# Kernel optimization log

Measured on AMD Instinct MI355X. Metric: run time of the kernel, lower is better.

Reference implementation:

```python
import jax, jax.numpy as jnp
import numpy as np
from jax import lax

B, N, D, OUT = 256, 4096, 512, 512
EPS = 1e-5
NPOINT = 128  # 4 modalities * 32 tokens each


def setup_inputs() -> dict:
    key = jax.random.key(0)
    ks = jax.random.split(key, 32)
    f32 = jnp.float32
    nrm = lambda k, s, sc=0.05: jax.random.normal(k, s, f32) * sc
    inp = {
        'rgb': jax.random.normal(ks[0], (B, 49, D), f32),
        'depth': jax.random.normal(ks[1], (B, 49, D), f32),
        'mmwave': jax.random.normal(ks[2], (B, 32, D), f32),
        'lidar': jax.random.normal(ks[3], (B, 32, D), f32),
        'lidar_points': jax.random.normal(ks[4], (B, N, 3), f32),
        # per-modality conv1d(k=1) weights, stacked [rgb, depth, mmwave, lidar]
        'conv_w': nrm(ks[5], (4, OUT, D)),
        'conv_b': nrm(ks[6], (4, OUT)),
        # eval-mode BatchNorm1d params per modality
        'bn_g': 1.0 + nrm(ks[7], (4, OUT)),
        'bn_b': nrm(ks[8], (4, OUT)),
        'bn_m': nrm(ks[9], (4, OUT)),
        'bn_v': 0.5 + jax.random.uniform(ks[10], (4, OUT), f32),
        # nn.Linear(49,32) for rgb/depth, nn.Linear(32,32) for mmwave/lidar
        'lin_w_img': nrm(ks[11], (2, 32, 49)),
        'lin_b_img': nrm(ks[12], (2, 32)),
        'lin_w_pc': nrm(ks[13], (2, 32, 32)),
        'lin_b_pc': nrm(ks[14], (2, 32)),
        # pos_enc_layer: Conv1d(3,128,1)+BN+ReLU, Conv1d(128,OUT,1)+BN+ReLU
        'pe_w1': nrm(ks[15], (128, 3)),
        'pe_b1': nrm(ks[16], (128,)),
        'pe_g1': 1.0 + nrm(ks[17], (128,)),
        'pe_bb1': nrm(ks[18], (128,)),
        'pe_m1': nrm(ks[19], (128,)),
        'pe_v1': 0.5 + jax.random.uniform(ks[20], (128,), f32),
        'pe_w2': nrm(ks[21], (OUT, 128)),
        'pe_b2': nrm(ks[22], (OUT,)),
        'pe_g2': 1.0 + nrm(ks[23], (OUT,)),
        'pe_bb2': nrm(ks[24], (OUT,)),
        'pe_m2': nrm(ks[25], (OUT,)),
        'pe_v2': 0.5 + jax.random.uniform(ks[26], (OUT,), f32),
    }
    return inp


def _bn(x, g, b, m, v):
    # x: [B, C, L]; eval-mode batchnorm over channel dim
    return (x - m[:, None]) * (g / jnp.sqrt(v + EPS))[:, None] + b[:, None]


def _branch(x, cw, cb, g, bb, m, v, lw, lb):
    # x: [B, L, D] (already the un-permuted feature); conv1d(k=1) == matmul
    h = jnp.einsum('bld,od->bol', x, cw) + cb[:, None]  # [B, OUT, L]
    h = jax.nn.relu(_bn(h, g, bb, m, v))
    h = jnp.einsum('bol,kl->bok', h, lw) + lb           # Linear on last dim -> [B, OUT, 32]
    return jax.nn.relu(h)


def _fps(xyz, npoint):
    # faithful farthest point sampling: npoint sequential iterations as lax.scan
    Bb, Nn, _ = xyz.shape
    far0 = jax.random.randint(jax.random.key(42), (Bb,), 0, Nn)
    dist0 = jnp.full((Bb, Nn), 1e10, xyz.dtype)
    def step(carry, _):
        distance, farthest = carry
        idx = jnp.broadcast_to(farthest[:, None, None], (Bb, 1, 3))
        centroid = jnp.take_along_axis(xyz, idx, axis=1)      # [B,1,3]
        d = jnp.sum((xyz - centroid) ** 2, -1)                # [B,N]
        distance = jnp.minimum(distance, d)
        return (distance, jnp.argmax(distance, -1)), farthest
    _, idxs = lax.scan(step, (dist0, far0), None, length=npoint)
    return jnp.transpose(idxs)  # [B, npoint]


def reference(rgb, depth, mmwave, lidar, lidar_points,
              conv_w, conv_b, bn_g, bn_b, bn_m, bn_v,
              lin_w_img, lin_b_img, lin_w_pc, lin_b_pc,
              pe_w1, pe_b1, pe_g1, pe_bb1, pe_m1, pe_v1,
              pe_w2, pe_b2, pe_g2, pe_bb2, pe_m2, pe_v2):
    # active_modalities = ['rgb','depth','mmwave','lidar']
    feats = [
        _branch(rgb,    conv_w[0], conv_b[0], bn_g[0], bn_b[0], bn_m[0], bn_v[0], lin_w_img[0], lin_b_img[0]),
        _branch(depth,  conv_w[1], conv_b[1], bn_g[1], bn_b[1], bn_m[1], bn_v[1], lin_w_img[1], lin_b_img[1]),
        _branch(mmwave, conv_w[2], conv_b[2], bn_g[2], bn_b[2], bn_m[2], bn_v[2], lin_w_pc[0], lin_b_pc[0]),
        _branch(lidar,  conv_w[3], conv_b[3], bn_g[3], bn_b[3], bn_m[3], bn_v[3], lin_w_pc[1], lin_b_pc[1]),
    ]
    proj = jnp.transpose(jnp.concatenate(feats, axis=2), (0, 2, 1))  # [B, 128, OUT]
    S = proj.shape[1]
    fps_idx = _fps(lidar_points, S)                                   # [B, S]
    gi = jnp.broadcast_to(fps_idx[..., None], (lidar_points.shape[0], S, 3))
    new_xyz = jnp.take_along_axis(lidar_points, gi, axis=1)           # [B, S, 3]
    h = jnp.einsum('bsd,od->bos', new_xyz, pe_w1) + pe_b1[:, None]    # [B,128,S]
    h = jax.nn.relu(_bn(h, pe_g1, pe_bb1, pe_m1, pe_v1))
    h = jnp.einsum('bcs,oc->bos', h, pe_w2) + pe_b2[:, None]          # [B,OUT,S]
    h = jax.nn.relu(_bn(h, pe_g2, pe_bb2, pe_m2, pe_v2))
    return proj + jnp.transpose(h, (0, 2, 1))
```

## Files before the change

### kernel.cpp

```cpp
#include <hip/hip_runtime.h>
#include <stdint.h>

typedef unsigned int u32;
typedef unsigned short u16;

typedef __attribute__((ext_vector_type(8))) short bf16x8;
typedef __attribute__((ext_vector_type(8))) unsigned short u16x8;
typedef __attribute__((ext_vector_type(4))) float f32x4;

__device__ __forceinline__ u16 f2bfu(float f) {
  union { float f; u32 u; } v; v.f = f;
  return (u16)((v.u + 0x7FFFu + ((v.u >> 16) & 1u)) >> 16);
}

__device__ __forceinline__ void gload16(const void* g, void* l) {
  __builtin_amdgcn_global_load_lds(
      (const __attribute__((address_space(1))) void*)g,
      (__attribute__((address_space(3))) void*)l, 16, 0, 0);
}

__device__ __forceinline__ u32 rotl32(u32 x, int r) { return (x << r) | (x >> (32 - r)); }

__device__ __forceinline__ uint2 threefry2x32(u32 k0, u32 k1, u32 x0, u32 x1) {
  u32 ks2 = k0 ^ k1 ^ 0x1BD11BDAu;
  x0 += k0; x1 += k1;
#define TF_G(a,b,c,d) { x0 += x1; x1 = rotl32(x1,a); x1 ^= x0; \
                        x0 += x1; x1 = rotl32(x1,b); x1 ^= x0; \
                        x0 += x1; x1 = rotl32(x1,c); x1 ^= x0; \
                        x0 += x1; x1 = rotl32(x1,d); x1 ^= x0; }
  TF_G(13,15,26,6);  x0 += k1;  x1 += ks2 + 1u;
  TF_G(17,29,16,24); x0 += ks2; x1 += k0  + 2u;
  TF_G(13,15,26,6);  x0 += k0;  x1 += k1  + 3u;
  TF_G(17,29,16,24); x0 += k1;  x1 += ks2 + 4u;
  TF_G(13,15,26,6);  x0 += ks2; x1 += k0  + 5u;
#undef TF_G
  return make_uint2(x0, x1);
}

__global__ __launch_bounds__(256) void convert_kernel(
    const float* __restrict__ rgb, const float* __restrict__ depth,
    const float* __restrict__ mmw, const float* __restrict__ lid,
    const float* __restrict__ conv_w, u16* __restrict__ Wc, u16* __restrict__ Xc)
{
  const int bid = blockIdx.x, tid = threadIdx.x;
  float4 v0 = make_float4(0.f, 0.f, 0.f, 0.f), v1 = v0;
  char* dst;
  if (bid < 12288) {
    const int y = bid >> 4, ks = bid & 15;
    const int l = tid >> 2, seg = tid & 3;
    const float* xp; size_t row = 0; bool valid = true;
    if (y < 256)      { xp = rgb;   row = (size_t)y * 49 + l;         valid = (l < 49); }
    else if (y < 512) { xp = depth; row = (size_t)(y - 256) * 49 + l; valid = (l < 49); }
    else if (y < 640) { xp = mmw;   row = (size_t)(y - 512) * 64 + l; }
    else              { xp = lid;   row = (size_t)(y - 640) * 64 + l; }
    if (valid) {
      const float* s = xp + row * 512 + ks * 32 + seg * 8;
      v0 = *(const float4*)s; v1 = *(const float4*)(s + 4);
    }
    dst = (char*)Xc + (size_t)y * 65536 + ks * 4096 + l * 64 + ((seg ^ ((l >> 1) & 3)) << 4);
  } else {
    const int t = bid - 12288;
    const int tile = t >> 1, half = t & 1;
    const int row = (tid >> 2) + half * 64, seg = tid & 3;
    const float* s = conv_w + (size_t)((tile >> 4) * 128 + row) * 512 + (tile & 15) * 32 + seg * 8;
    v0 = *(const float4*)s; v1 = *(const float4*)(s + 4);
    dst = (char*)Wc + (size_t)tile * 8192 + row * 64 + ((seg ^ ((row >> 1) & 3)) << 4);
  }
  u16x8 pk;
  pk[0] = f2bfu(v0.x); pk[1] = f2bfu(v0.y); pk[2] = f2bfu(v0.z); pk[3] = f2bfu(v0.w);
  pk[4] = f2bfu(v1.x); pk[5] = f2bfu(v1.y); pk[6] = f2bfu(v1.z); pk[7] = f2bfu(v1.w);
  *(u16x8*)dst = pk;
}

#define FSMEM_SZ 52864

__global__ __launch_bounds__(256) void fused_kernel(
    const float* __restrict__ pts, int* __restrict__ fps_idx,
    const u16* __restrict__ Wc, const u16* __restrict__ Xc,
    const float* __restrict__ conv_b,
    const float* __restrict__ bn_g, const float* __restrict__ bn_b,
    const float* __restrict__ bn_m, const float* __restrict__ bn_v,
    const float* __restrict__ lin_w_img, const float* __restrict__ lin_b_img,
    const float* __restrict__ lin_w_pc, const float* __restrict__ lin_b_pc,
    float* __restrict__ out)
{
  __shared__ __align__(16) char sm[FSMEM_SZ];
  const int tid = threadIdx.x;

  if (blockIdx.x < 256) {
    float* xs = (float*)sm;
    float* ys = (float*)(sm + 16384);
    float* zs = (float*)(sm + 32768);
    float* rv2 = (float*)(sm + 49152);
    int*   ri2 = (int*)(sm + 49184);
    const int b = blockIdx.x;
    const float* pb = pts + (size_t)b * 4096 * 3;

    __builtin_amdgcn_s_setprio(1);

    for (int i = tid; i < 12288; i += 256) {
      float v = pb[i];
      int n = i / 3, c = i - n * 3;
      float* dstp = (c == 0) ? xs : (c == 1) ? ys : zs;
      dstp[n] = v;
    }
    __syncthreads();

    float xr[16], yr[16], zr[16], dreg[16];
#pragma unroll
    for (int i = 0; i < 16; i++) {
      int n = tid + (i << 8);
      xr[i] = xs[n]; yr[i] = ys[n]; zr[i] = zs[n];
      dreg[i] = 1e10f;
    }

    uint2 k2 = threefry2x32(0u, 42u, 0u, 1u);
    uint2 r  = threefry2x32(k2.x, k2.y, 0u, (u32)b);
    int far  = (int)((r.x ^ r.y) & 4095u);
    const int wv = tid >> 6;

    for (int s = 0; s < 128; s++) {
      if (tid == 0) fps_idx[b * 128 + s] = far;
      float cx = xs[far], cy = ys[far], cz = zs[far];
      float bv[16]; int bn[16];
#pragma unroll
      for (int i = 0; i < 16; i++) {
        float dx = __fsub_rn(xr[i], cx);
        float dy = __fsub_rn(yr[i], cy);
        float dz = __fsub_rn(zr[i], cz);
        float d  = __fadd_rn(__fadd_rn(__fmul_rn(dx, dx), __fmul_rn(dy, dy)), __fmul_rn(dz, dz));
        float nd = fminf(dreg[i], d);
        dreg[i] = nd;
        bv[i] = nd; bn[i] = tid + (i << 8);
      }
#define MRG(i, j) if (bv[j] > bv[i]) { bv[i] = bv[j]; bn[i] = bn[j]; }
      MRG(0, 8)  MRG(1, 9)  MRG(2, 10) MRG(3, 11)
      MRG(4, 12) MRG(5, 13) MRG(6, 14) MRG(7, 15)
      MRG(0, 4)  MRG(1, 5)  MRG(2, 6)  MRG(3, 7)
      MRG(0, 2)  MRG(1, 3)
      MRG(0, 1)
#undef MRG
      float bestv = bv[0]; int besti = bn[0];
#pragma unroll
      for (int off = 1; off < 64; off <<= 1) {
        float ov = __shfl_xor(bestv, off, 64);
        int   oi = __shfl_xor(besti, off, 64);
        if (ov > bestv || (ov == bestv && oi < besti)) { bestv = ov; besti = oi; }
      }
      const int par = s & 1;
      if ((tid & 63) == 0) { rv2[par * 4 + wv] = bestv; ri2[par * 4 + wv] = besti; }
      __syncthreads();
      float bvv = rv2[par * 4]; int bii = ri2[par * 4];
#pragma unroll
      for (int w2 = 1; w2 < 4; w2++) {
        float wvv = rv2[par * 4 + w2]; int wii = ri2[par * 4 + w2];
        if (wvv > bvv || (wvv == bvv && wii < bii)) { bvv = wvv; bii = wii; }
      }
      far = bii;
    }
    return;
  }

  const int g  = (int)blockIdx.x - 256;
  const int ot = g & 3;
  const int y  = g >> 2;
  int mod, bidx = 0, bg = 0;
  if      (y < 256) { mod = 0; bidx = y; }
  else if (y < 512) { mod = 1; bidx = y - 256; }
  else if (y < 640) { mod = 2; bg   = y - 512; }
  else              { mod = 3; bg   = y - 640; }
  const bool img = (mod < 2);
  const int  L   = img ? 49 : 32;
  const float* lw = img ? (lin_w_img + mod * 32 * 49) : (lin_w_pc + (mod - 2) * 32 * 32);
  const float* lb = img ? (lin_b_img + mod * 32)      : (lin_b_pc + (mod - 2) * 32);

  u16*   lw2 = (u16*)(sm + 47104);
  float* bnA = (float*)(sm + 51712);
  float* bnC = (float*)(sm + 52224);
  float* lbs = (float*)(sm + 52736);
  u16*   hsB = (u16*)(sm + 24576);
  float* Cb  = (float*)sm;

  for (int i = tid; i < 32 * 64; i += 256) {
    int kk = i >> 6, l = i & 63;
    float v = (l < L) ? lw[kk * L + l] : 0.f;
    lw2[kk * 72 + l] = f2bfu(v);
  }
  if (tid < 32) lbs[tid] = lb[tid];
  if (tid < 128) {
    int o = mod * 512 + ot * 128 + tid;
    float sc = bn_g[o] / sqrtf(bn_v[o] + 1e-5f);
    bnA[tid] = sc;
    bnC[tid] = (conv_b[o] - bn_m[o]) * sc + bn_b[o];
  }

  const int lane = tid & 63, w = tid >> 6, quad = lane >> 4, lm = lane & 15;
  const int xorq = ((lm >> 1) & 3) << 4;
  const int soff = w * 1024 + lane * 16;

  const char* wcB = (const char*)Wc + (size_t)(mod * 4 + ot) * (16 * 8192);
  const char* xcB = (const char*)Xc + (size_t)y * 65536;

  f32x4 acc[2][4];
#pragma unroll
  for (int mi = 0; mi < 2; mi++)
#pragma unroll
    for (int nt = 0; nt < 4; nt++) acc[mi][nt] = (f32x4){0.f, 0.f, 0.f, 0.f};

  asm volatile("s_waitcnt vmcnt(0)" ::: "memory");
  gload16(wcB + soff,        sm + soff);
  gload16(wcB + soff + 4096, sm + soff + 4096);
  gload16(xcB + soff,        sm + 16384 + soff);

#pragma unroll
  for (int ks = 0; ks < 16; ks++) {
    const int cur = ks & 1;
    if (ks < 15) {
      const char* wsrc = wcB + (ks + 1) * 8192;
      const char* xsrc = xcB + (ks + 1) * 4096;
      char* wd = sm + (cur ^ 1) * 8192;
      char* xd = sm + 16384 + (cur ^ 1) * 4096;
      gload16(wsrc + soff,        wd + soff);
      gload16(wsrc + soff + 4096, wd + soff + 4096);
      gload16(xsrc + soff,        xd + soff);
      asm volatile("s_waitcnt vmcnt(3)" ::: "memory");
    } else {
      asm volatile("s_waitcnt vmcnt(0)" ::: "memory");
    }
    __builtin_amdgcn_s_barrier();
    asm volatile("" ::: "memory");
    const char* wbc = sm + cur * 8192;
    const char* xbc = sm + 16384 + cur * 4096;
    bf16x8 af[2], bfr[4];
#pragma unroll
    for (int mi = 0; mi < 2; mi++)
      af[mi] = *(const bf16x8*)(wbc + w * 2048 + mi * 1024 + lm * 64 + ((quad * 16) ^ xorq));
#pragma unroll
    for (int nt = 0; nt < 4; nt++)
      bfr[nt] = *(const bf16x8*)(xbc + nt * 1024 + lm * 64 + ((quad * 16) ^ xorq));
#pragma unroll
    for (int mi = 0; mi < 2; mi++)
#pragma unroll
      for (int nt = 0; nt < 4; nt++)
        acc[mi][nt] = __builtin_amdgcn_mfma_f32_16x16x32_bf16(af[mi], bfr[nt], acc[mi][nt], 0, 0, 0);
    asm volatile("s_waitcnt lgkmcnt(0)" ::: "memory");
    __builtin_amdgcn_s_barrier();
  }

#pragma unroll
  for (int mi = 0; mi < 2; mi++)
#pragma unroll
    for (int nt = 0; nt < 4; nt++)
#pragma unroll
      for (int r = 0; r < 4; r++) {
        int o_loc = w * 32 + mi * 16 + quad * 4 + r;
        int l     = nt * 16 + lm;
        float v = acc[mi][nt][r] * bnA[o_loc] + bnC[o_loc];
        hsB[o_loc * 88 + l] = f2bfu(v > 0.f ? v : 0.f);
      }
  __syncthreads();

  const int npass = img ? 1 : 2;
  const int nkt   = img ? 2 : 1;
  for (int p = 0; p < npass; p++) {
    f32x4 c2[2][2];
#pragma unroll
    for (int mi = 0; mi < 2; mi++)
#pragma unroll
      for (int nt2 = 0; nt2 < 2; nt2++) c2[mi][nt2] = (f32x4){0.f, 0.f, 0.f, 0.f};
    for (int kt = 0; kt < nkt; kt++) {
      int aoff = img ? kt * 32 : p * 32;
      int boff = img ? kt * 32 : 0;
      bf16x8 a2[2], b2[2];
#pragma unroll
      for (int mi = 0; mi < 2; mi++)
        a2[mi] = *(const bf16x8*)&hsB[(w * 32 + mi * 16 + lm) * 88 + aoff + quad * 8];
#pragma unroll
      for (int nt2 = 0; nt2 < 2; nt2++)
        b2[nt2] = *(const bf16x8*)&lw2[(nt2 * 16 + lm) * 72 + boff + quad * 8];
#pragma unroll
      for (int mi = 0; mi < 2; mi++)
#pragma unroll
        for (int nt2 = 0; nt2 < 2; nt2++)
          c2[mi][nt2] = __builtin_amdgcn_mfma_f32_16x16x32_bf16(a2[mi], b2[nt2], c2[mi][nt2], 0, 0, 0);
    }
#pragma unroll
    for (int mi = 0; mi < 2; mi++)
#pragma unroll
      for (int nt2 = 0; nt2 < 2; nt2++)
#pragma unroll
        for (int r = 0; r < 4; r++) {
          int kk    = nt2 * 16 + lm;
          int o_loc = w * 32 + mi * 16 + quad * 4 + r;
          float v = c2[mi][nt2][r] + lbs[kk];
          Cb[kk * 132 + o_loc] = v > 0.f ? v : 0.f;
        }
    __syncthreads();
    int b_out = img ? bidx : (bg * 2 + p);
    for (int i = tid; i < 4096; i += 256) {
      int kk = i >> 7, j = i & 127;
      out[((size_t)b_out * 128 + mod * 32 + kk) * 512 + ot * 128 + j] = Cb[kk * 132 + j];
    }
    if (p + 1 < npass) __syncthreads();
  }
}

#define WB_OFF   0
#define XB_OFF   8192
#define CB_OFF   0
#define HS_OFF   16896
#define LW2_OFF  39424
#define BNA_OFF  44032
#define BNC_OFF  44544
#define LBS_OFF  45056
#define SMEM_SZ  45184

__global__ __launch_bounds__(256) void branch_kernel(
    const float* __restrict__ x0p, const float* __restrict__ x1p,
    const float* __restrict__ x2p, const float* __restrict__ x3p,
    const float* __restrict__ conv_w, const float* __restrict__ conv_b,
    const float* __restrict__ bn_g, const float* __restrict__ bn_b,
    const float* __restrict__ bn_m, const float* __restrict__ bn_v,
    const float* __restrict__ lin_w_img, const float* __restrict__ lin_b_img,
    const float* __restrict__ lin_w_pc, const float* __restrict__ lin_b_pc,
    float* __restrict__ out)
{
  __shared__ __align__(16) char sm[SMEM_SZ];
  u16*   Wb  = (u16*)(sm + WB_OFF);
  u16*   Xb  = (u16*)(sm + XB_OFF);
  float* Cb  = (float*)(sm + CB_OFF);
  u16*   hsB = (u16*)(sm + HS_OFF);
  u16*   lw2 = (u16*)(sm + LW2_OFF);
  float* bnA = (float*)(sm + BNA_OFF);
  float* bnC = (float*)(sm + BNC_OFF);
  float* lbs = (float*)(sm + LBS_OFF);

  const int ot  = blockIdx.x;
  const int tid = threadIdx.x;
  int y = blockIdx.y;
  int mod, bidx = 0, bg = 0;
  if      (y < 256) { mod = 0; bidx = y; }
  else if (y < 512) { mod = 1; bidx = y - 256; }
  else if (y < 640) { mod = 2; bg   = y - 512; }
  else              { mod = 3; bg   = y - 640; }
  const bool img = (mod < 2);
  const int  L   = img ? 49 : 32;
  const float* xp = (mod == 0) ? x0p : (mod == 1) ? x1p : (mod == 2) ? x2p : x3p;
  const float* lw = img ? (lin_w_img + mod * 32 * 49) : (lin_w_pc + (mod - 2) * 32 * 32);
  const float* lb = img ? (lin_b_img + mod * 32)      : (lin_b_pc + (mod - 2) * 32);

  for (int i = tid; i < 32 * 64; i += 256) {
    int kk = i >> 6, l = i & 63;
    float v = (l < L) ? lw[kk * L + l] : 0.f;
    lw2[kk * 72 + l] = f2bfu(v);
  }
  if (tid < 32) lbs[tid] = lb[tid];
  if (tid < 128) {
    int o = mod * 512 + ot * 128 + tid;
    float sc = bn_g[o] / sqrtf(bn_v[o] + 1e-5f);
    bnA[tid] = sc;
    bnC[tid] = (conv_b[o] - bn_m[o]) * sc + bn_b[o];
  }

  const int lane = tid & 63, w = tid >> 6, quad = lane >> 4, lm = lane & 15;
  const float* wbase = conv_w + (size_t)(mod * 512 + ot * 128) * 512;

  f32x4 acc[2][4];
#pragma unroll
  for (int mi = 0; mi < 2; mi++)
#pragma unroll
    for (int nt = 0; nt < 4; nt++) acc[mi][nt] = (f32x4){0.f, 0.f, 0.f, 0.f};

  for (int ks = 0; ks < 16; ks++) {
    int k0 = ks * 32;
    __syncthreads();
    for (int i = tid; i < 1024; i += 256) {
      int row = i >> 3, seg = i & 7;
      float4 v = *(const float4*)(wbase + (size_t)row * 512 + k0 + seg * 4);
      u16* d = &Wb[row * 32 + seg * 4];
      d[0] = f2bfu(v.x); d[1] = f2bfu(v.y); d[2] = f2bfu(v.z); d[3] = f2bfu(v.w);
    }
    for (int i = tid; i < 512; i += 256) {
      int l = i >> 3, seg = i & 7;
      float4 v = make_float4(0.f, 0.f, 0.f, 0.f);
      if (img) {
        if (l < 49) v = *(const float4*)(xp + (size_t)(bidx * 49 + l) * 512 + k0 + seg * 4);
      } else {
        v = *(const float4*)(xp + (size_t)(bg * 64 + l) * 512 + k0 + seg * 4);
      }
      u16* d = &Xb[l * 32 + seg * 4];
      d[0] = f2bfu(v.x); d[1] = f2bfu(v.y); d[2] = f2bfu(v.z); d[3] = f2bfu(v.w);
    }
    __syncthreads();
    bf16x8 af[2], bfr[4];
#pragma unroll
    for (int mi = 0; mi < 2; mi++)
      af[mi] = *(const bf16x8*)&Wb[(w * 32 + mi * 16 + lm) * 32 + quad * 8];
#pragma unroll
    for (int nt = 0; nt < 4; nt++)
      bfr[nt] = *(const bf16x8*)&Xb[(nt * 16 + lm) * 32 + quad * 8];
#pragma unroll
    for (int mi = 0; mi < 2; mi++)
#pragma unroll
      for (int nt = 0; nt < 4; nt++)
        acc[mi][nt] = __builtin_amdgcn_mfma_f32_16x16x32_bf16(af[mi], bfr[nt], acc[mi][nt], 0, 0, 0);
  }
  __syncthreads();

#pragma unroll
  for (int mi = 0; mi < 2; mi++)
#pragma unroll
    for (int nt = 0; nt < 4; nt++)
#pragma unroll
      for (int r = 0; r < 4; r++) {
        int o_loc = w * 32 + mi * 16 + quad * 4 + r;
        int l     = nt * 16 + lm;
        float v = acc[mi][nt][r] * bnA[o_loc] + bnC[o_loc];
        hsB[o_loc * 88 + l] = f2bfu(v > 0.f ? v : 0.f);
      }
  __syncthreads();

  const int npass = img ? 1 : 2;
  const int nkt   = img ? 2 : 1;
  for (int p = 0; p < npass; p++) {
    f32x4 c2[2][2];
#pragma unroll
    for (int mi = 0; mi < 2; mi++)
#pragma unroll
      for (int nt2 = 0; nt2 < 2; nt2++) c2[mi][nt2] = (f32x4){0.f, 0.f, 0.f, 0.f};
    for (int kt = 0; kt < nkt; kt++) {
      int aoff = img ? kt * 32 : p * 32;
      int boff = img ? kt * 32 : 0;
      bf16x8 a2[2], b2[2];
#pragma unroll
      for (int mi = 0; mi < 2; mi++)
        a2[mi] = *(const bf16x8*)&hsB[(w * 32 + mi * 16 + lm) * 88 + aoff + quad * 8];
#pragma unroll
      for (int nt2 = 0; nt2 < 2; nt2++)
        b2[nt2] = *(const bf16x8*)&lw2[(nt2 * 16 + lm) * 72 + boff + quad * 8];
#pragma unroll
      for (int mi = 0; mi < 2; mi++)
#pragma unroll
        for (int nt2 = 0; nt2 < 2; nt2++)
          c2[mi][nt2] = __builtin_amdgcn_mfma_f32_16x16x32_bf16(a2[mi], b2[nt2], c2[mi][nt2], 0, 0, 0);
    }
#pragma unroll
    for (int mi = 0; mi < 2; mi++)
#pragma unroll
      for (int nt2 = 0; nt2 < 2; nt2++)
#pragma unroll
        for (int r = 0; r < 4; r++) {
          int kk    = nt2 * 16 + lm;
          int o_loc = w * 32 + mi * 16 + quad * 4 + r;
          float v = c2[mi][nt2][r] + lbs[kk];
          Cb[kk * 132 + o_loc] = v > 0.f ? v : 0.f;
        }
    __syncthreads();
    int b_out = img ? bidx : (bg * 2 + p);
    for (int i = tid; i < 4096; i += 256) {
      int kk = i >> 7, j = i & 127;
      out[((size_t)b_out * 128 + mod * 32 + kk) * 512 + ot * 128 + j] = Cb[kk * 132 + j];
    }
    if (p + 1 < npass) __syncthreads();
  }
}

__global__ __launch_bounds__(256) void fps_kernel(const float* __restrict__ pts,
                                                  int* __restrict__ idx_out)
{
  __shared__ float xs[4096], ys[4096], zs[4096];
  __shared__ float rv[4];
  __shared__ int   ri[4];
  __shared__ int   far_sh;
  const int b = blockIdx.x, tid = threadIdx.x;
  const float* pb = pts + (size_t)b * 4096 * 3;

  for (int i = tid; i < 12288; i += 256) {
    float v = pb[i];
    int n = i / 3, c = i - n * 3;
    float* dst = (c == 0) ? xs : (c == 1) ? ys : zs;
    dst[n] = v;
  }
  float dreg[16];
#pragma unroll
  for (int i = 0; i < 16; i++) dreg[i] = 1e10f;
  __syncthreads();

  uint2 k2 = threefry2x32(0u, 42u, 0u, 1u);
  uint2 r  = threefry2x32(k2.x, k2.y, 0u, (u32)b);
  int far  = (int)((r.x ^ r.y) & 4095u);

  for (int s = 0; s < 128; s++) {
    if (tid == 0) idx_out[b * 128 + s] = far;
    float cx = xs[far], cy = ys[far], cz = zs[far];
    float bestv = -1.f; int besti = 0x7FFFFFFF;
#pragma unroll
    for (int i = 0; i < 16; i++) {
      int n = tid + (i << 8);
      float dx = __fsub_rn(xs[n], cx);
      float dy = __fsub_rn(ys[n], cy);
      float dz = __fsub_rn(zs[n], cz);
      float d  = __fadd_rn(__fadd_rn(__fmul_rn(dx, dx), __fmul_rn(dy, dy)), __fmul_rn(dz, dz));
      float nd = fminf(dreg[i], d);
      dreg[i] = nd;
      if (nd > bestv) { bestv = nd; besti = n; }
    }
#pragma unroll
    for (int off = 1; off < 64; off <<= 1) {
      float ov = __shfl_xor(bestv, off, 64);
      int   oi = __shfl_xor(besti, off, 64);
      if (ov > bestv || (ov == bestv && oi < besti)) { bestv = ov; besti = oi; }
    }
    if ((tid & 63) == 0) { rv[tid >> 6] = bestv; ri[tid >> 6] = besti; }
    __syncthreads();
    if (tid == 0) {
      float bv = rv[0]; int bi = ri[0];
#pragma unroll
      for (int w = 1; w < 4; w++)
        if (rv[w] > bv || (rv[w] == bv && ri[w] < bi)) { bv = rv[w]; bi = ri[w]; }
      far_sh = bi;
    }
    __syncthreads();
    far = far_sh;
  }
}

__global__ __launch_bounds__(256) void pe_kernel(
    const float* __restrict__ pts, const int* __restrict__ fps_idx,
    const float* __restrict__ w1, const float* __restrict__ b1,
    const float* __restrict__ g1, const float* __restrict__ bb1,
    const float* __restrict__ m1, const float* __restrict__ v1,
    const float* __restrict__ w2, const float* __restrict__ b2,
    const float* __restrict__ g2, const float* __restrict__ bb2,
    const float* __restrict__ m2, const float* __restrict__ v2,
    float* __restrict__ out)
{
  __shared__ float h1T[64][132];
  __shared__ float w2s[64][132];
  __shared__ float sc1s[128], C1s[128];
  const int ot = blockIdx.x;
  const int st = blockIdx.y;
  const int b  = blockIdx.z;
  const int tid = threadIdx.x;

  for (int i = tid; i < 64 * 32; i += 256) {
    int o = i >> 5, j = i & 31;
    float4 v = *(const float4*)(w2 + (size_t)(ot * 64 + o) * 128 + j * 4);
    *(float4*)&w2s[o][j * 4] = v;
  }
  if (tid < 128) {
    float sc = g1[tid] / sqrtf(v1[tid] + 1e-5f);
    sc1s[tid] = sc;
    C1s[tid]  = (b1[tid] - m1[tid]) * sc + bb1[tid];
  }
  __syncthreads();

  {
    int s_l = tid & 63;
    int cq  = tid >> 6;
    int s   = st * 64 + s_l;
    int n   = fps_idx[b * 128 + s];
    float px = pts[((size_t)b * 4096 + n) * 3 + 0];
    float py = pts[((size_t)b * 4096 + n) * 3 + 1];
    float pz = pts[((size_t)b * 4096 + n) * 3 + 2];
    for (int cc = 0; cc < 32; cc++) {
      int c = cq * 32 + cc;
      float d  = fmaf(pz, w1[c * 3 + 2], fmaf(py, w1[c * 3 + 1], px * w1[c * 3]));
      float h  = d * sc1s[c] + C1s[c];
      h1T[s_l][c] = h > 0.f ? h : 0.f;
    }
  }
  __syncthreads();

  const int tx = tid & 15, ty = tid >> 4;
  float acc[4][4];
#pragma unroll
  for (int j = 0; j < 4; j++)
#pragma unroll
    for (int i = 0; i < 4; i++) acc[j][i] = 0.f;

  for (int c = 0; c < 128; c += 4) {
    float4 wv[4];
#pragma unroll
    for (int j = 0; j < 4; j++) wv[j] = *(const float4*)&w2s[tx + 16 * j][c];
#pragma unroll
    for (int si = 0; si < 4; si++) {
      float4 hv = *(const float4*)&h1T[ty + 16 * si][c];
#pragma unroll
      for (int j = 0; j < 4; j++) {
        acc[j][si] = fmaf(hv.x, wv[j].x, acc[j][si]);
        acc[j][si] = fmaf(hv.y, wv[j].y, acc[j][si]);
        acc[j][si] = fmaf(hv.z, wv[j].z, acc[j][si]);
        acc[j][si] = fmaf(hv.w, wv[j].w, acc[j][si]);
      }
    }
  }

#pragma unroll
  for (int j = 0; j < 4; j++) {
    int o = ot * 64 + tx + 16 * j;
    float sc = g2[o] / sqrtf(v2[o] + 1e-5f);
    float C  = (b2[o] - m2[o]) * sc + bb2[o];
#pragma unroll
    for (int si = 0; si < 4; si++) {
      int s = st * 64 + ty + 16 * si;
      float v = acc[j][si] * sc + C;
      v = v > 0.f ? v : 0.f;
      size_t oi = ((size_t)b * 128 + s) * 512 + o;
      out[oi] = out[oi] + v;
    }
  }
}

extern "C" void kernel_launch(void* const* d_in, const int* in_sizes, int n_in,
                              void* d_out, int out_size, void* d_ws, size_t ws_size,
                              hipStream_t stream) {
  const float* rgb    = (const float*)d_in[0];
  const float* depth  = (const float*)d_in[1];
  const float* mmwave = (const float*)d_in[2];
  const float* lidar  = (const float*)d_in[3];
  const float* pts    = (const float*)d_in[4];
  const float* conv_w = (const float*)d_in[5];
  const float* conv_b = (const float*)d_in[6];
  const float* bn_g   = (const float*)d_in[7];
  const float* bn_b   = (const float*)d_in[8];
  const float* bn_m   = (const float*)d_in[9];
  const float* bn_v   = (const float*)d_in[10];
  const float* lwi    = (const float*)d_in[11];
  const float* lbi    = (const float*)d_in[12];
  const float* lwp    = (const float*)d_in[13];
  const float* lbp    = (const float*)d_in[14];
  const float* pw1    = (const float*)d_in[15];
  const float* pb1    = (const float*)d_in[16];
  const float* pg1    = (const float*)d_in[17];
  const float* pbb1   = (const float*)d_in[18];
  const float* pm1    = (const float*)d_in[19];
  const float* pv1    = (const float*)d_in[20];
  const float* pw2    = (const float*)d_in[21];
  const float* pb2    = (const float*)d_in[22];
  const float* pg2    = (const float*)d_in[23];
  const float* pbb2   = (const float*)d_in[24];
  const float* pm2    = (const float*)d_in[25];
  const float* pv2    = (const float*)d_in[26];
  float* out = (float*)d_out;
  int* fps_idx = (int*)d_ws;

  const size_t NEED = 131072 + 2097152 + (size_t)768 * 65536;
  if (ws_size >= NEED) {
    u16* Wc = (u16*)((char*)d_ws + 131072);
    u16* Xc = (u16*)((char*)d_ws + 2228224);
    convert_kernel<<<dim3(12800), 256, 0, stream>>>(rgb, depth, mmwave, lidar,
        conv_w, Wc, Xc);
    fused_kernel<<<dim3(3328), 256, 0, stream>>>(pts, fps_idx, Wc, Xc,
        conv_b, bn_g, bn_b, bn_m, bn_v, lwi, lbi, lwp, lbp, out);
  } else {
    branch_kernel<<<dim3(4, 768), 256, 0, stream>>>(rgb, depth, mmwave, lidar,
        conv_w, conv_b, bn_g, bn_b, bn_m, bn_v, lwi, lbi, lwp, lbp, out);
    fps_kernel<<<dim3(256), 256, 0, stream>>>(pts, fps_idx);
  }
  pe_kernel<<<dim3(8, 2, 256), 256, 0, stream>>>(pts, fps_idx, pw1, pb1, pg1, pbb1, pm1, pv1,
      pw2, pb2, pg2, pbb2, pm2, pv2, out);
}
```

Before: 444.7 us.

## Move positional-encoding MLP to split-bf16 MFMA and use DPP for FPS argmax

Replaces the scalar positional-encoding kernel with an MFMA kernel. It splits the hidden activations and the second-layer weights into hi/lo bf16 pairs and does three bf16 MFMAs per tile to stay close to fp32 accuracy. The convert kernel now also precomputes the hi/lo weights and the folded BN scale/shift vectors. The FPS wave-level argmax reduction swaps shuffle-xor for DPP row ops plus a readlane, to cut latency on the serial FPS critical path. This adds workspace use and a 3x MFMA count.

```diff
diff --git a/kernel.cpp b/kernel.cpp
--- a/kernel.cpp
+++ b/kernel.cpp
@@ -11,12 +11,25 @@
 __device__ __forceinline__ u16 f2bfu(float f) {
   union { float f; u32 u; } v; v.f = f;
   return (u16)((v.u + 0x7FFFu + ((v.u >> 16) & 1u)) >> 16);
+}
+__device__ __forceinline__ float bf2f(u16 h) {
+  union { u32 u; float f; } v; v.u = ((u32)h) << 16;
+  return v.f;
 }
 
 __device__ __forceinline__ void gload16(const void* g, void* l) {
   __builtin_amdgcn_global_load_lds(
       (const __attribute__((address_space(1))) void*)g,
       (__attribute__((address_space(3))) void*)l, 16, 0, 0);
+}
+
+template <int CTRL>
+__device__ __forceinline__ void dpp_merge(float& bv, int& bi) {
+  int ovi = __builtin_amdgcn_update_dpp(__float_as_int(bv), __float_as_int(bv),
+                                        CTRL, 0xF, 0xF, false);
+  int oii = __builtin_amdgcn_update_dpp(bi, bi, CTRL, 0xF, 0xF, false);
+  float ov = __int_as_float(ovi);
+  if (ov > bv || (ov == bv && oii < bi)) { bv = ov; bi = oii; }
 }
 
 __device__ __forceinline__ u32 rotl32(u32 x, int r) { return (x << r) | (x >> (32 - r)); }
@@ -40,12 +53,20 @@
 __global__ __launch_bounds__(256) void convert_kernel(
     const float* __restrict__ rgb, const float* __restrict__ depth,
     const float* __restrict__ mmw, const float* __restrict__ lid,
-    const float* __restrict__ conv_w, u16* __restrict__ Wc, u16* __restrict__ Xc)
+    const float* __restrict__ conv_w, u16* __restrict__ Wc, u16* __restrict__ Xc,
+    const float* __restrict__ pw2,
+    const float* __restrict__ pg1, const float* __restrict__ pbb1,
+    const float* __restrict__ pm1, const float* __restrict__ pv1,
+    const float* __restrict__ pb1,
+    const float* __restrict__ pg2, const float* __restrict__ pbb2,
+    const float* __restrict__ pm2, const float* __restrict__ pv2,
+    const float* __restrict__ pb2,
+    u16* __restrict__ W2h, u16* __restrict__ W2l,
+    float* __restrict__ sc1C1, float* __restrict__ sc2C2)
 {
   const int bid = blockIdx.x, tid = threadIdx.x;
-  float4 v0 = make_float4(0.f, 0.f, 0.f, 0.f), v1 = v0;
-  char* dst;
   if (bid < 12288) {
+    float4 v0 = make_float4(0.f, 0.f, 0.f, 0.f), v1 = v0;
     const int y = bid >> 4, ks = bid & 15;
     const int l = tid >> 2, seg = tid & 3;
     const float* xp; size_t row = 0; bool valid = true;
@@ -57,19 +78,48 @@
       const float* s = xp + row * 512 + ks * 32 + seg * 8;
       v0 = *(const float4*)s; v1 = *(const float4*)(s + 4);
     }
-    dst = (char*)Xc + (size_t)y * 65536 + ks * 4096 + l * 64 + ((seg ^ ((l >> 1) & 3)) << 4);
-  } else {
+    char* dst = (char*)Xc + (size_t)y * 65536 + ks * 4096 + l * 64 + ((seg ^ ((l >> 1) & 3)) << 4);
+    u16x8 pk;
+    pk[0] = f2bfu(v0.x); pk[1] = f2bfu(v0.y); pk[2] = f2bfu(v0.z); pk[3] = f2bfu(v0.w);
+    pk[4] = f2bfu(v1.x); pk[5] = f2bfu(v1.y); pk[6] = f2bfu(v1.z); pk[7] = f2bfu(v1.w);
+    *(u16x8*)dst = pk;
+  } else if (bid < 12800) {
     const int t = bid - 12288;
     const int tile = t >> 1, half = t & 1;
     const int row = (tid >> 2) + half * 64, seg = tid & 3;
     const float* s = conv_w + (size_t)((tile >> 4) * 128 + row) * 512 + (tile & 15) * 32 + seg * 8;
-    v0 = *(const float4*)s; v1 = *(const float4*)(s + 4);
-    dst = (char*)Wc + (size_t)tile * 8192 + row * 64 + ((seg ^ ((row >> 1) & 3)) << 4);
-  }
-  u16x8 pk;
-  pk[0] = f2bfu(v0.x); pk[1] = f2bfu(v0.y); pk[2] = f2bfu(v0.z); pk[3] = f2bfu(v0.w);
-  pk[4] = f2bfu(v1.x); pk[5] = f2bfu(v1.y); pk[6] = f2bfu(v1.z); pk[7] = f2bfu(v1.w);
-  *(u16x8*)dst = pk;
+    float4 v0 = *(const float4*)s; float4 v1 = *(const float4*)(s + 4);
+    char* dst = (char*)Wc + (size_t)tile * 8192 + row * 64 + ((seg ^ ((row >> 1) & 3)) << 4);
+    u16x8 pk;
+    pk[0] = f2bfu(v0.x); pk[1] = f2bfu(v0.y); pk[2] = f2bfu(v0.z); pk[3] = f2bfu(v0.w);
+    pk[4] = f2bfu(v1.x); pk[5] = f2bfu(v1.y); pk[6] = f2bfu(v1.z); pk[7] = f2bfu(v1.w);
+    *(u16x8*)dst = pk;
+  } else if (bid < 12832) {
+    const int idx = (bid - 12800) * 2048 + tid * 8;
+    const float* s = pw2 + idx;
+    float4 v0 = *(const float4*)s; float4 v1 = *(const float4*)(s + 4);
+    float vv[8] = {v0.x, v0.y, v0.z, v0.w, v1.x, v1.y, v1.z, v1.w};
+    u16x8 hh, hl;
+#pragma unroll
+    for (int j = 0; j < 8; j++) {
+      u16 hi = f2bfu(vv[j]);
+      hh[j] = hi;
+      hl[j] = f2bfu(vv[j] - bf2f(hi));
+    }
+    *(u16x8*)(W2h + idx) = hh;
+    *(u16x8*)(W2l + idx) = hl;
+  } else {
+    if (tid < 128) {
+      float sc = pg1[tid] / sqrtf(pv1[tid] + 1e-5f);
+      sc1C1[tid]       = sc;
+      sc1C1[128 + tid] = (pb1[tid] - pm1[tid]) * sc + pbb1[tid];
+    }
+    for (int o = tid; o < 512; o += 256) {
+      float sc = pg2[o] / sqrtf(pv2[o] + 1e-5f);
+      sc2C2[o]       = sc;
+      sc2C2[512 + o] = (pb2[o] - pm2[o]) * sc + pbb2[o];
+    }
+  }
 }
 
 #define FSMEM_SZ 52864
@@ -141,14 +191,17 @@
       MRG(0, 1)
 #undef MRG
       float bestv = bv[0]; int besti = bn[0];
-#pragma unroll
-      for (int off = 1; off < 64; off <<= 1) {
-        float ov = __shfl_xor(bestv, off, 64);
-        int   oi = __shfl_xor(besti, off, 64);
-        if (ov > bestv || (ov == bestv && oi < besti)) { bestv = ov; besti = oi; }
-      }
+      dpp_merge<0x111>(bestv, besti);
+      dpp_merge<0x112>(bestv, besti);
+      dpp_merge<0x114>(bestv, besti);
+      dpp_merge<0x118>(bestv, besti);
+      dpp_merge<0x142>(bestv, besti);
+      dpp_merge<0x143>(bestv, besti);
+      float wbv = __int_as_float(__builtin_amdgcn_readlane(__float_as_int(bestv), 63));
+      int   wbi = __builtin_amdgcn_readlane(besti, 63);
+
       const int par = s & 1;
-      if ((tid & 63) == 0) { rv2[par * 4 + wv] = bestv; ri2[par * 4 + wv] = besti; }
+      if ((tid & 63) == 0) { rv2[par * 4 + wv] = wbv; ri2[par * 4 + wv] = wbi; }
       __syncthreads();
       float bvv = rv2[par * 4]; int bii = ri2[par * 4];
 #pragma unroll
@@ -302,6 +355,97 @@
       out[((size_t)b_out * 128 + mod * 32 + kk) * 512 + ot * 128 + j] = Cb[kk * 132 + j];
     }
     if (p + 1 < npass) __syncthreads();
+  }
+}
+
+__global__ __launch_bounds__(256) void pe_mfma_kernel(
+    const float* __restrict__ pts, const int* __restrict__ fps_idx,
+    const float* __restrict__ w1,
+    const u16* __restrict__ W2h, const u16* __restrict__ W2l,
+    const float* __restrict__ sc1C1, const float* __restrict__ sc2C2,
+    float* __restrict__ out)
+{
+  __shared__ __align__(16) char sm[65536];
+  u16* Ph = (u16*)sm;
+  u16* Pl = (u16*)(sm + 16384);
+  u16* Wh = (u16*)(sm + 32768);
+  u16* Wl = (u16*)(sm + 49152);
+  const int ot = blockIdx.x;
+  const int st = blockIdx.y;
+  const int b  = blockIdx.z;
+  const int tid = threadIdx.x;
+
+  for (int i = tid; i < 1024; i += 256) {
+    int o = i >> 4, gn = i & 15;
+    u16x8 vh = *(const u16x8*)(W2h + ((size_t)(ot * 64 + o)) * 128 + gn * 8);
+    u16x8 vl = *(const u16x8*)(W2l + ((size_t)(ot * 64 + o)) * 128 + gn * 8);
+    int gg = gn ^ (o & 15);
+    *(u16x8*)(Wh + o * 128 + gg * 8) = vh;
+    *(u16x8*)(Wl + o * 128 + gg * 8) = vl;
+  }
+  {
+    int s_l = tid >> 2;
+    int cq  = (tid & 3) * 32;
+    int s   = st * 64 + s_l;
+    int n   = fps_idx[b * 128 + s];
+    float px = pts[((size_t)b * 4096 + n) * 3 + 0];
+    float py = pts[((size_t)b * 4096 + n) * 3 + 1];
+    float pz = pts[((size_t)b * 4096 + n) * 3 + 2];
+    for (int c0 = 0; c0 < 32; c0 += 8) {
+      u16x8 hh, hl;
+#pragma unroll
+      for (int j = 0; j < 8; j++) {
+        int c = cq + c0 + j;
+        float d = fmaf(pz, w1[c * 3 + 2], fmaf(py, w1[c * 3 + 1], px * w1[c * 3]));
+        float h = d * sc1C1[c] + sc1C1[128 + c];
+        h = h > 0.f ? h : 0.f;
+        u16 hi = f2bfu(h);
+        hh[j] = hi;
+        hl[j] = f2bfu(h - bf2f(hi));
+      }
+      int gn = (cq + c0) >> 3;
+      int gg = gn ^ (s_l & 15);
+      *(u16x8*)(Ph + s_l * 128 + gg * 8) = hh;
+      *(u16x8*)(Pl + s_l * 128 + gg * 8) = hl;
+    }
+  }
+  __syncthreads();
+
+  const int lane = tid & 63, w = tid >> 6, quad = lane >> 4, lm = lane & 15;
+  f32x4 acc[4];
+#pragma unroll
+  for (int nt = 0; nt < 4; nt++) acc[nt] = (f32x4){0.f, 0.f, 0.f, 0.f};
+
+  const int arow = w * 16 + lm;
+#pragma unroll
+  for (int kt = 0; kt < 4; kt++) {
+    int ag = ((kt * 4 + quad) ^ (arow & 15)) * 8;
+    bf16x8 pah = *(const bf16x8*)(Ph + arow * 128 + ag);
+    bf16x8 pal = *(const bf16x8*)(Pl + arow * 128 + ag);
+#pragma unroll
+    for (int nt = 0; nt < 4; nt++) {
+      int brow = nt * 16 + lm;
+      int bg = ((kt * 4 + quad) ^ (brow & 15)) * 8;
+      bf16x8 wbh = *(const bf16x8*)(Wh + brow * 128 + bg);
+      bf16x8 wbl = *(const bf16x8*)(Wl + brow * 128 + bg);
+      acc[nt] = __builtin_amdgcn_mfma_f32_16x16x32_bf16(pah, wbh, acc[nt], 0, 0, 0);
+      acc[nt] = __builtin_amdgcn_mfma_f32_16x16x32_bf16(pah, wbl, acc[nt], 0, 0, 0);
+      acc[nt] = __builtin_amdgcn_mfma_f32_16x16x32_bf16(pal, wbh, acc[nt], 0, 0, 0);
+    }
+  }
+
+#pragma unroll
+  for (int nt = 0; nt < 4; nt++) {
+    int o = ot * 64 + nt * 16 + lm;
+    float sc = sc2C2[o], C = sc2C2[512 + o];
+#pragma unroll
+    for (int r = 0; r < 4; r++) {
+      int s = st * 64 + w * 16 + quad * 4 + r;
+      float v = acc[nt][r] * sc + C;
+      v = v > 0.f ? v : 0.f;
+      size_t oi = ((size_t)b * 128 + s) * 512 + o;
+      out[oi] = out[oi] + v;
+    }
   }
 }
 
@@ -645,19 +789,32 @@
   float* out = (float*)d_out;
   int* fps_idx = (int*)d_ws;
 
-  const size_t NEED = 131072 + 2097152 + (size_t)768 * 65536;
+  const size_t O_WC   = 131072;
+  const size_t O_XC   = 2228224;
+  const size_t O_W2H  = 52559872;
+  const size_t O_W2L  = 52690944;
+  const size_t O_SC1  = 52822016;
+  const size_t O_SC2  = 52823040;
+  const size_t NEED   = 52827136;
   if (ws_size >= NEED) {
-    u16* Wc = (u16*)((char*)d_ws + 131072);
-    u16* Xc = (u16*)((char*)d_ws + 2228224);
-    convert_kernel<<<dim3(12800), 256, 0, stream>>>(rgb, depth, mmwave, lidar,
-        conv_w, Wc, Xc);
+    u16*   Wc    = (u16*)((char*)d_ws + O_WC);
+    u16*   Xc    = (u16*)((char*)d_ws + O_XC);
+    u16*   W2h   = (u16*)((char*)d_ws + O_W2H);
+    u16*   W2l   = (u16*)((char*)d_ws + O_W2L);
+    float* sc1C1 = (float*)((char*)d_ws + O_SC1);
+    float* sc2C2 = (float*)((char*)d_ws + O_SC2);
+    convert_kernel<<<dim3(12833), 256, 0, stream>>>(rgb, depth, mmwave, lidar,
+        conv_w, Wc, Xc, pw2, pg1, pbb1, pm1, pv1, pb1, pg2, pbb2, pm2, pv2, pb2,
+        W2h, W2l, sc1C1, sc2C2);
     fused_kernel<<<dim3(3328), 256, 0, stream>>>(pts, fps_idx, Wc, Xc,
         conv_b, bn_g, bn_b, bn_m, bn_v, lwi, lbi, lwp, lbp, out);
+    pe_mfma_kernel<<<dim3(8, 2, 256), 256, 0, stream>>>(pts, fps_idx, pw1,
+        W2h, W2l, sc1C1, sc2C2, out);
   } else {
     branch_kernel<<<dim3(4, 768), 256, 0, stream>>>(rgb, depth, mmwave, lidar,
         conv_w, conv_b, bn_g, bn_b, bn_m, bn_v, lwi, lbi, lwp, lbp, out);
     fps_kernel<<<dim3(256), 256, 0, stream>>>(pts, fps_idx);
-  }
-  pe_kernel<<<dim3(8, 2, 256), 256, 0, stream>>>(pts, fps_idx, pw1, pb1, pg1, pbb1, pm1, pv1,
-      pw2, pb2, pg2, pbb2, pm2, pv2, out);
-}
+    pe_kernel<<<dim3(8, 2, 256), 256, 0, stream>>>(pts, fps_idx, pw1, pb1, pg1, pbb1, pm1, pv1,
+        pw2, pb2, pg2, pbb2, pm2, pv2, out);
+  }
+}
```

Result: faster. 430.0 us (-3.3%).
